# Kernel tuning notes

Hardware: AMD Instinct MI355X
Metric: run time of the kernel (lower is better)

## Reference

```python
import jax, jax.numpy as jnp
import numpy as np

D_MODEL = 1024
N_HEADS = 16
D_HEAD = D_MODEL // N_HEADS
D_FF = 4096
B, T = 2, 2048


def setup_inputs() -> dict:
    key = jax.random.key(0)
    ks = jax.random.split(key, 8)
    s = 0.02
    return {
        "x": jax.random.normal(ks[0], (B, T, D_MODEL), dtype=jnp.float32),
        "wq": jax.random.normal(ks[1], (D_MODEL, D_MODEL), dtype=jnp.float32) * s,
        "wk": jax.random.normal(ks[2], (D_MODEL, D_MODEL), dtype=jnp.float32) * s,
        "wv": jax.random.normal(ks[3], (D_MODEL, D_MODEL), dtype=jnp.float32) * s,
        "wo": jax.random.normal(ks[4], (D_MODEL, D_MODEL), dtype=jnp.float32) * s,
        "w1": jax.random.normal(ks[5], (D_FF, D_MODEL), dtype=jnp.float32) * s,
        "b1": jnp.zeros((D_FF,), dtype=jnp.float32),
        "w2": jax.random.normal(ks[6], (D_MODEL, D_FF), dtype=jnp.float32) * s,
        "b2": jnp.zeros((D_MODEL,), dtype=jnp.float32),
        "ln1_g": jnp.ones((D_MODEL,), dtype=jnp.float32),
        "ln1_b": jnp.zeros((D_MODEL,), dtype=jnp.float32),
        "ln2_g": jnp.ones((D_MODEL,), dtype=jnp.float32),
        "ln2_b": jnp.zeros((D_MODEL,), dtype=jnp.float32),
    }


def _layernorm(x, g, b, eps=1e-5):
    mu = jnp.mean(x, axis=-1, keepdims=True)
    var = jnp.mean(jnp.square(x - mu), axis=-1, keepdims=True)
    return (x - mu) * jax.lax.rsqrt(var + eps) * g + b


def reference(x, wq, wk, wv, wo, w1, b1, w2, b2, ln1_g, ln1_b, ln2_g, ln2_b):
    Bsz, Tlen, C = x.shape
    h = _layernorm(x, ln1_g, ln1_b)
    # torch Linear: y = h @ W^T ; reshape to [B, H, T, Dh]
    def proj(w):
        return (h @ w.T).reshape(Bsz, Tlen, N_HEADS, D_HEAD).transpose(0, 2, 1, 3)
    q, k, v = proj(wq), proj(wk), proj(wv)
    scores = jnp.einsum('bhqd,bhkd->bhqk', q, k) / np.sqrt(D_HEAD).astype(np.float32)
    p = jax.nn.softmax(scores.astype(jnp.float32), axis=-1).astype(scores.dtype)
    out = jnp.einsum('bhqk,bhkd->bhqd', p, v)
    out = out.transpose(0, 2, 1, 3).reshape(Bsz, Tlen, C)
    x = x + out @ wo.T
    h2 = _layernorm(x, ln2_g, ln2_b)
    ff = jax.nn.gelu(h2 @ w1.T + b1, approximate=False) @ w2.T + b2
    return x + ff
```

## Files before the change

kernel.cpp:

```cpp
#include <hip/hip_runtime.h>
#include <hip/hip_bf16.h>
#include <math.h>

#define DM   1024
#define NH   16
#define DH   64
#define DFF  4096
#define BB   2
#define TT   2048
#define MTOK (BB*TT)
#define QS   3072

typedef unsigned short u16;
typedef unsigned int   u32;
typedef __attribute__((ext_vector_type(8))) __bf16 bf16x8;
typedef __attribute__((ext_vector_type(4))) float  f32x4;

__device__ inline float bf2f(u16 u) { return __uint_as_float(((u32)u) << 16); }
__device__ inline u16 f2bf(float f) {
  u32 u = __float_as_uint(f);
  u += 0x7FFFu + ((u >> 16) & 1u);
  return (u16)(u >> 16);
}
__device__ inline u32 packtrunc(float lo, float hi) {
  return __builtin_amdgcn_perm(__float_as_uint(hi), __float_as_uint(lo), 0x07060302u);
}
__device__ inline float fexp2(float x) { return __builtin_amdgcn_exp2f(x); }

__device__ inline void gload_lds16(const void* g, void* l) {
  __builtin_amdgcn_global_load_lds(
      (const __attribute__((address_space(1))) void*)g,
      (__attribute__((address_space(3))) void*)l,
      16, 0, 0);
}

__global__ __launch_bounds__(256) void prep(
    const float* __restrict__ wq, const float* __restrict__ wk, const float* __restrict__ wv,
    const float* __restrict__ wo, const float* __restrict__ w1, const float* __restrict__ w2,
    const float* __restrict__ x, const float* __restrict__ g, const float* __restrict__ be,
    u16* __restrict__ wqkv_b, u16* __restrict__ wo_b, u16* __restrict__ w1_b,
    u16* __restrict__ w2_b, u16* __restrict__ h1)
{
  const int blk = blockIdx.x;
  if (blk < 12288) {
    const float* src; u16* dst; int idx;
    if (blk < 3072) {
      idx = blk * 256 + threadIdx.x;
      const int sel = idx >> 18;
      const int j = idx & 0x3FFFF;
      src = sel == 0 ? wq : (sel == 1 ? wk : wv);
      dst = wqkv_b;
      float4 v = ((const float4*)src)[j];
      ushort4 o; o.x = f2bf(v.x); o.y = f2bf(v.y); o.z = f2bf(v.z); o.w = f2bf(v.w);
      ((ushort4*)dst)[idx] = o;
      return;
    } else if (blk < 4096) { src = wo; dst = wo_b; idx = (blk - 3072) * 256 + threadIdx.x; }
    else if (blk < 8192)   { src = w1; dst = w1_b; idx = (blk - 4096) * 256 + threadIdx.x; }
    else                   { src = w2; dst = w2_b; idx = (blk - 8192) * 256 + threadIdx.x; }
    float4 v = ((const float4*)src)[idx];
    ushort4 o; o.x = f2bf(v.x); o.y = f2bf(v.y); o.z = f2bf(v.z); o.w = f2bf(v.w);
    ((ushort4*)dst)[idx] = o;
    return;
  }
  const int w = threadIdx.x >> 6, lane = threadIdx.x & 63;
  const int row = (blk - 12288) * 4 + w;
  const float4* xr = (const float4*)(x + (size_t)row * DM);
  float4 v[4];
  float s = 0.f, s2 = 0.f;
#pragma unroll
  for (int i = 0; i < 4; i++) {
    v[i] = xr[i * 64 + lane];
    s  += v[i].x + v[i].y + v[i].z + v[i].w;
    s2 += v[i].x * v[i].x + v[i].y * v[i].y + v[i].z * v[i].z + v[i].w * v[i].w;
  }
#pragma unroll
  for (int off = 32; off > 0; off >>= 1) {
    s  += __shfl_xor(s,  off);
    s2 += __shfl_xor(s2, off);
  }
  const float mu = s * (1.f / DM);
  const float rs = rsqrtf(s2 * (1.f / DM) - mu * mu + 1e-5f);
  u16* orow = h1 + (size_t)row * DM;
#pragma unroll
  for (int i = 0; i < 4; i++) {
    const float4 gg = ((const float4*)g)[i * 64 + lane];
    const float4 bb = ((const float4*)be)[i * 64 + lane];
    ushort4 o;
    o.x = f2bf((v[i].x - mu) * rs * gg.x + bb.x);
    o.y = f2bf((v[i].y - mu) * rs * gg.y + bb.y);
    o.z = f2bf((v[i].z - mu) * rs * gg.z + bb.z);
    o.w = f2bf((v[i].w - mu) * rs * gg.w + bb.w);
    ((ushort4*)orow)[i * 64 + lane] = o;
  }
}

__global__ __launch_bounds__(256) void ln_to_bf16(
    const float* __restrict__ x, const float* __restrict__ g, const float* __restrict__ be,
    u16* __restrict__ out)
{
  const int w = threadIdx.x >> 6, lane = threadIdx.x & 63;
  const int row = blockIdx.x * 4 + w;
  const float4* xr = (const float4*)(x + (size_t)row * DM);
  float4 v[4];
  float s = 0.f, s2 = 0.f;
#pragma unroll
  for (int i = 0; i < 4; i++) {
    v[i] = xr[i * 64 + lane];
    s  += v[i].x + v[i].y + v[i].z + v[i].w;
    s2 += v[i].x * v[i].x + v[i].y * v[i].y + v[i].z * v[i].z + v[i].w * v[i].w;
  }
#pragma unroll
  for (int off = 32; off > 0; off >>= 1) {
    s  += __shfl_xor(s,  off);
    s2 += __shfl_xor(s2, off);
  }
  const float mu = s * (1.f / DM);
  const float rs = rsqrtf(s2 * (1.f / DM) - mu * mu + 1e-5f);
  u16* orow = out + (size_t)row * DM;
#pragma unroll
  for (int i = 0; i < 4; i++) {
    const float4 gg = ((const float4*)g)[i * 64 + lane];
    const float4 bb = ((const float4*)be)[i * 64 + lane];
    ushort4 o;
    o.x = f2bf((v[i].x - mu) * rs * gg.x + bb.x);
    o.y = f2bf((v[i].y - mu) * rs * gg.y + bb.y);
    o.z = f2bf((v[i].z - mu) * rs * gg.z + bb.z);
    o.w = f2bf((v[i].w - mu) * rs * gg.w + bb.w);
    ((ushort4*)orow)[i * 64 + lane] = o;
  }
}

template <int EPI, int BN>
__global__ __launch_bounds__(256) void gemm_bt(
    const u16* __restrict__ A, const u16* __restrict__ Bw,
    int M, int N, int K,
    const float* __restrict__ bias, const float* __restrict__ resid,
    float* __restrict__ outF, u16* __restrict__ outB, float oscale, int scaleN)
{
  constexpr int NJ = BN / 32;
  __shared__ u16 As[128 * 64];
  __shared__ u16 Bs[BN * 64];

  const int tid  = threadIdx.x;
  const int w    = tid >> 6;
  const int lane = tid & 63;
  const int wr   = w >> 1, wc = w & 1;
  const int q    = lane >> 4;
  const int li   = lane & 15;
  const int rowBase = blockIdx.y * 128;
  const int colBase = blockIdx.x * BN;

  const int lr = lane >> 3;
  const int cs = (lane & 7) ^ lr;
  const u16* Abase = A  + (size_t)(rowBase + lr) * K + cs * 8;
  const u16* Bbase = Bw + (size_t)(colBase + lr) * K + cs * 8;

  f32x4 acc[4][NJ] = {};

  for (int k0 = 0; k0 < K; k0 += 64) {
    __syncthreads();
#pragma unroll
    for (int jj = 0; jj < 4; jj++) {
      const int rb = (w * 4 + jj) * 8;
      gload_lds16(Abase + (size_t)rb * K + k0, &As[rb * 64]);
    }
#pragma unroll
    for (int jj = 0; jj < NJ; jj++) {
      const int rb = (w * NJ + jj) * 8;
      gload_lds16(Bbase + (size_t)rb * K + k0, &Bs[rb * 64]);
    }
    __syncthreads();
#pragma unroll
    for (int kk = 0; kk < 2; kk++) {
      bf16x8 fa[4], fb[NJ];
      const int pos = (kk * 4 + q) ^ (li & 7);
#pragma unroll
      for (int i = 0; i < 4; i++) {
        const int row = wr * 64 + i * 16 + li;
        fa[i] = *(const bf16x8*)&As[row * 64 + pos * 8];
      }
#pragma unroll
      for (int j = 0; j < NJ; j++) {
        const int row = wc * (BN / 2) + j * 16 + li;
        fb[j] = *(const bf16x8*)&Bs[row * 64 + pos * 8];
      }
#pragma unroll
      for (int i = 0; i < 4; i++)
#pragma unroll
        for (int j = 0; j < NJ; j++)
          acc[i][j] = __builtin_amdgcn_mfma_f32_16x16x32_bf16(fa[i], fb[j], acc[i][j], 0, 0, 0);
    }
  }

#pragma unroll
  for (int i = 0; i < 4; i++) {
#pragma unroll
    for (int j = 0; j < NJ; j++) {
      const int col = colBase + wc * (BN / 2) + j * 16 + li;
      float bv = 0.f;
      if constexpr (EPI == 2 || EPI == 3) bv = bias[col];
#pragma unroll
      for (int r = 0; r < 4; r++) {
        const int row = rowBase + wr * 64 + i * 16 + q * 4 + r;
        float v = acc[i][j][r] + bv;
        if constexpr (EPI == 1 || EPI == 3) v += resid[(size_t)row * N + col];
        if constexpr (EPI == 2) {
          const float z = fexp2(-v * (2.302213f + 0.1029625f * v * v));
          v = v * __builtin_amdgcn_rcpf(1.f + z);
        }
        if constexpr (EPI == 0) {
          const float sc = (col < scaleN) ? oscale : 1.f;
          v *= sc;
        }
        if constexpr (EPI == 0 || EPI == 2) outB[(size_t)row * N + col] = f2bf(v);
        else                                outF[(size_t)row * N + col] = v;
      }
    }
  }
}

__global__ __launch_bounds__(256) void transpose_v(
    const u16* __restrict__ vq, u16* __restrict__ vt)
{
  __shared__ u16 t[64][72];
  const int bh = blockIdx.x, b = bh >> 4, h = bh & 15;
  const int t0 = blockIdx.y * 64;
  const int tid = threadIdx.x;
  const int r = tid >> 2, c = (tid & 3) * 16;
  const u16* src = vq + (size_t)(b * TT + t0 + r) * QS + h * DH + c;
#pragma unroll
  for (int i = 0; i < 4; i++)
    *(ushort4*)&t[r][c + i * 4] = ((const ushort4*)src)[i];
  __syncthreads();
  const int dh = tid >> 2, tt = (tid & 3) * 16;
  u16* dst = vt + ((size_t)bh * 64 + dh) * TT + t0 + tt;
#pragma unroll
  for (int i = 0; i < 4; i++) {
    ushort4 o;
    o.x = t[tt + i * 4 + 0][dh]; o.y = t[tt + i * 4 + 1][dh];
    o.z = t[tt + i * 4 + 2][dh]; o.w = t[tt + i * 4 + 3][dh];
    ((ushort4*)dst)[i] = o;
  }
}

__global__ __launch_bounds__(256) void attn_mfma(
    const u16* __restrict__ qb, const u16* __restrict__ kb,
    const u16* __restrict__ vt, u16* __restrict__ ob)
{
  __shared__ u16 Ks[2][64 * 64];
  __shared__ u16 Vs[2][64 * 64];
  __shared__ u16 Sh[4 * 32 * 72];

  const int tid = threadIdx.x, w = tid >> 6, lane = tid & 63;
  const int q = lane >> 4, li = lane & 15;
  const int bh = blockIdx.x, b = bh >> 4, h = bh & 15;
  const int q0 = blockIdx.y * 128;
  const int lr8 = lane >> 3, lc8 = lane & 7;

#pragma unroll
  for (int jj = 0; jj < 4; jj++) {
    const int rb = w * 32 + jj * 8;
    const int row = rb + lr8;
    const int cs = lc8 ^ (row & 7);
    gload_lds16(qb + (size_t)(b * TT + q0 + row) * QS + h * DH + cs * 8,
                &Sh[rb * 64]);
  }
  __syncthreads();

  bf16x8 qf[2][2];
#pragma unroll
  for (int n = 0; n < 2; n++)
#pragma unroll
    for (int kk = 0; kk < 2; kk++) {
      const int row = w * 32 + n * 16 + li;
      const int pos = (kk * 4 + q) ^ (li & 7);
      qf[n][kk] = *(const bf16x8*)&Sh[row * 64 + pos * 8];
    }

  auto stage = [&](int buf, int kt) {
#pragma unroll
    for (int half = 0; half < 2; half++) {
      const int rb = w * 16 + half * 8;
      const int row = rb + lr8;
      const int cs = lc8 ^ (row & 7);
      gload_lds16(kb + (size_t)(b * TT + kt + row) * QS + h * DH + cs * 8,
                  &Ks[buf][rb * 64]);
      gload_lds16(vt + ((size_t)bh * 64 + row) * TT + kt + cs * 8,
                  &Vs[buf][rb * 64]);
    }
  };

  f32x4 ot[4][2] = {};
  float lsum[2] = {0.f, 0.f};
  u16* Pw = &Sh[w * 32 * 72];

  stage(0, 0);
  for (int it = 0; it < TT / 64; it++) {
    __syncthreads();
    if (it + 1 < TT / 64) stage((it + 1) & 1, (it + 1) * 64);
    const u16* Kc = Ks[it & 1];
    const u16* Vc = Vs[it & 1];

    f32x4 st[4][2] = {};
#pragma unroll
    for (int kk = 0; kk < 2; kk++)
#pragma unroll
      for (int i = 0; i < 4; i++) {
        const int pos = (kk * 4 + q) ^ (li & 7);
        const bf16x8 kf = *(const bf16x8*)&Kc[(i * 16 + li) * 64 + pos * 8];
#pragma unroll
        for (int n = 0; n < 2; n++)
          st[i][n] = __builtin_amdgcn_mfma_f32_16x16x32_bf16(kf, qf[n][kk], st[i][n], 0, 0, 0);
      }

    u32 pk[4][2][2];
#pragma unroll
    for (int i = 0; i < 4; i++)
#pragma unroll
      for (int n = 0; n < 2; n++) {
        const float p0 = fexp2(st[i][n][0]);
        const float p1 = fexp2(st[i][n][1]);
        const float p2 = fexp2(st[i][n][2]);
        const float p3 = fexp2(st[i][n][3]);
        lsum[n] += (p0 + p1) + (p2 + p3);
        pk[i][n][0] = packtrunc(p0, p1);
        pk[i][n][1] = packtrunc(p2, p3);
      }

#pragma unroll
    for (int i = 0; i < 4; i++)
#pragma unroll
      for (int n = 0; n < 2; n++) {
        const int a = (n * 16 + li) * 72 + i * 16 + q * 4;
        *(u32*)&Pw[a]     = pk[i][n][0];
        *(u32*)&Pw[a + 2] = pk[i][n][1];
      }

#pragma unroll
    for (int kk = 0; kk < 2; kk++) {
      bf16x8 pf[2];
#pragma unroll
      for (int n = 0; n < 2; n++)
        pf[n] = *(const bf16x8*)&Pw[(n * 16 + li) * 72 + kk * 32 + q * 8];
#pragma unroll
      for (int m = 0; m < 4; m++) {
        const int pos = (kk * 4 + q) ^ (li & 7);
        const bf16x8 vf = *(const bf16x8*)&Vc[(m * 16 + li) * 64 + pos * 8];
#pragma unroll
        for (int n = 0; n < 2; n++)
          ot[m][n] = __builtin_amdgcn_mfma_f32_16x16x32_bf16(vf, pf[n], ot[m][n], 0, 0, 0);
      }
    }
  }

  float inv[2];
#pragma unroll
  for (int n = 0; n < 2; n++) {
    float s = lsum[n];
    s += __shfl_xor(s, 16);
    s += __shfl_xor(s, 32);
    inv[n] = 1.f / s;
  }
#pragma unroll
  for (int m = 0; m < 4; m++)
#pragma unroll
    for (int n = 0; n < 2; n++) {
      const int a = (n * 16 + li) * 72 + m * 16 + q * 4;
      *(u32*)&Pw[a]     = packtrunc(ot[m][n][0] * inv[n], ot[m][n][1] * inv[n]);
      *(u32*)&Pw[a + 2] = packtrunc(ot[m][n][2] * inv[n], ot[m][n][3] * inv[n]);
    }
#pragma unroll
  for (int pass = 0; pass < 4; pass++) {
    const int row = pass * 8 + lr8;
    const bf16x8 v = *(const bf16x8*)&Pw[row * 72 + lc8 * 8];
    const int token = q0 + w * 32 + row;
    *(bf16x8*)(ob + ((size_t)(b * TT + token) * NH + h) * DH + lc8 * 8) = v;
  }
}

extern "C" void kernel_launch(void* const* d_in, const int* in_sizes, int n_in,
                              void* d_out, int out_size, void* d_ws, size_t ws_size,
                              hipStream_t stream) {
  const float* x    = (const float*)d_in[0];
  const float* wq   = (const float*)d_in[1];
  const float* wk   = (const float*)d_in[2];
  const float* wv   = (const float*)d_in[3];
  const float* wo   = (const float*)d_in[4];
  const float* w1   = (const float*)d_in[5];
  const float* b1   = (const float*)d_in[6];
  const float* w2   = (const float*)d_in[7];
  const float* b2   = (const float*)d_in[8];
  const float* ln1g = (const float*)d_in[9];
  const float* ln1b = (const float*)d_in[10];
  const float* ln2g = (const float*)d_in[11];
  const float* ln2b = (const float*)d_in[12];

  size_t off = 0;
  char* base = (char*)d_ws;
  auto alloc = [&](size_t bytes) { void* p = base + off; off += bytes; return p; };

  u16* wqkv_b = (u16*)alloc((size_t)3 * DM * DM * 2);
  u16* wo_b   = (u16*)alloc((size_t)DM * DM * 2);
  u16* w1_b   = (u16*)alloc((size_t)DFF * DM * 2);
  u16* w2_b   = (u16*)alloc((size_t)DM * DFF * 2);
  u16* h1     = (u16*)alloc((size_t)MTOK * DM * 2);
  u16* qkvb   = (u16*)alloc((size_t)MTOK * QS * 2);
  u16* attn   = (u16*)alloc((size_t)MTOK * DM * 2);
  u16* h2     = (u16*)alloc((size_t)MTOK * DM * 2);
  u16* ff1    = (u16*)alloc((size_t)MTOK * DFF * 2);
  float* xmid = (float*)alloc((size_t)MTOK * DM * 4);
  u16* vtb    = ff1;
  (void)ws_size; (void)in_sizes; (void)n_in; (void)out_size;

  prep<<<13312, 256, 0, stream>>>(wq, wk, wv, wo, w1, w2, x, ln1g, ln1b,
                                  wqkv_b, wo_b, w1_b, w2_b, h1);

  const float QSCALE = 0.125f * 1.44269504088896340736f;
  gemm_bt<0, 128><<<dim3(QS / 128, MTOK / 128), 256, 0, stream>>>(
      h1, wqkv_b, MTOK, QS, DM, nullptr, nullptr, nullptr, qkvb, QSCALE, DM);

  transpose_v<<<dim3(BB * NH, TT / 64), 256, 0, stream>>>(qkvb + 2 * DM, vtb);
  attn_mfma<<<dim3(BB * NH, TT / 128), 256, 0, stream>>>(qkvb, qkvb + DM, vtb, attn);

  gemm_bt<1, 64><<<dim3(DM / 64, MTOK / 128), 256, 0, stream>>>(
      attn, wo_b, MTOK, DM, DM, nullptr, x, xmid, nullptr, 1.f, 0);

  ln_to_bf16<<<MTOK / 4, 256, 0, stream>>>(xmid, ln2g, ln2b, h2);

  gemm_bt<2, 128><<<dim3(DFF / 128, MTOK / 128), 256, 0, stream>>>(
      h2, w1_b, MTOK, DFF, DM, b1, nullptr, nullptr, ff1, 1.f, 0);
  gemm_bt<3, 64><<<dim3(DM / 64, MTOK / 128), 256, 0, stream>>>(
      ff1, w2_b, MTOK, DM, DFF, b2, xmid, (float*)d_out, nullptr, 1.f, 0);
}
```

Before: 355.5 us.

## Double-buffer GEMM LDS tiles with K-step 32 and one barrier per iteration

```diff
diff --git a/kernel.cpp b/kernel.cpp
--- a/kernel.cpp
+++ b/kernel.cpp
@@ -138,8 +138,8 @@
     float* __restrict__ outF, u16* __restrict__ outB, float oscale, int scaleN)
 {
   constexpr int NJ = BN / 32;
-  __shared__ u16 As[128 * 64];
-  __shared__ u16 Bs[BN * 64];
+  __shared__ u16 As[2][128 * 32];
+  __shared__ u16 Bs[2][BN * 32];
 
   const int tid  = threadIdx.x;
   const int w    = tid >> 6;
@@ -150,46 +150,64 @@
   const int rowBase = blockIdx.y * 128;
   const int colBase = blockIdx.x * BN;
 
-  const int lr = lane >> 3;
-  const int cs = (lane & 7) ^ lr;
-  const u16* Abase = A  + (size_t)(rowBase + lr) * K + cs * 8;
-  const u16* Bbase = Bw + (size_t)(colBase + lr) * K + cs * 8;
+  const int lrow = lane >> 2;
+  const int lchk = lane & 3;
+
+  const u16* Asrc[2];
+  const u16* Bsrc[NJ / 2 > 0 ? NJ / 2 : 1];
+  int Abase_lds[2], Bbase_lds[2];
+#pragma unroll
+  for (int jj = 0; jj < 2; jj++) {
+    const int row = w * 32 + jj * 16 + lrow;
+    const int cs = lchk ^ ((row >> 1) & 3);
+    Asrc[jj] = A + (size_t)(rowBase + row) * K + cs * 8;
+    Abase_lds[jj] = (w * 32 + jj * 16) * 32;
+  }
+#pragma unroll
+  for (int jj = 0; jj < NJ / 2; jj++) {
+    const int row = w * (16 * NJ / 2) + jj * 16 + lrow;
+    const int cs = lchk ^ ((row >> 1) & 3);
+    Bsrc[jj] = Bw + (size_t)(colBase + row) * K + cs * 8;
+    Bbase_lds[jj] = (w * (16 * NJ / 2) + jj * 16) * 32;
+  }
+
+  auto stage = [&](int buf, int k0) {
+#pragma unroll
+    for (int jj = 0; jj < 2; jj++)
+      gload_lds16(Asrc[jj] + k0, &As[buf][Abase_lds[jj]]);
+#pragma unroll
+    for (int jj = 0; jj < NJ / 2; jj++)
+      gload_lds16(Bsrc[jj] + k0, &Bs[buf][Bbase_lds[jj]]);
+  };
 
   f32x4 acc[4][NJ] = {};
 
-  for (int k0 = 0; k0 < K; k0 += 64) {
+  stage(0, 0);
+  const int NIT = K / 32;
+  for (int it = 0; it < NIT; it++) {
     __syncthreads();
-#pragma unroll
-    for (int jj = 0; jj < 4; jj++) {
-      const int rb = (w * 4 + jj) * 8;
-      gload_lds16(Abase + (size_t)rb * K + k0, &As[rb * 64]);
-    }
-#pragma unroll
-    for (int jj = 0; jj < NJ; jj++) {
-      const int rb = (w * NJ + jj) * 8;
-      gload_lds16(Bbase + (size_t)rb * K + k0, &Bs[rb * 64]);
-    }
-    __syncthreads();
-#pragma unroll
-    for (int kk = 0; kk < 2; kk++) {
-      bf16x8 fa[4], fb[NJ];
-      const int pos = (kk * 4 + q) ^ (li & 7);
-#pragma unroll
-      for (int i = 0; i < 4; i++) {
-        const int row = wr * 64 + i * 16 + li;
-        fa[i] = *(const bf16x8*)&As[row * 64 + pos * 8];
-      }
-#pragma unroll
-      for (int j = 0; j < NJ; j++) {
-        const int row = wc * (BN / 2) + j * 16 + li;
-        fb[j] = *(const bf16x8*)&Bs[row * 64 + pos * 8];
-      }
-#pragma unroll
-      for (int i = 0; i < 4; i++)
-#pragma unroll
-        for (int j = 0; j < NJ; j++)
-          acc[i][j] = __builtin_amdgcn_mfma_f32_16x16x32_bf16(fa[i], fb[j], acc[i][j], 0, 0, 0);
-    }
+    if (it + 1 < NIT) stage((it + 1) & 1, (it + 1) * 32);
+    const u16* Ac = As[it & 1];
+    const u16* Bc = Bs[it & 1];
+
+    bf16x8 fa[4], fb[NJ];
+#pragma unroll
+    for (int i = 0; i < 4; i++) {
+      const int row = wr * 64 + i * 16 + li;
+      const int pos = q ^ ((row >> 1) & 3);
+      fa[i] = *(const bf16x8*)&Ac[row * 32 + pos * 8];
+    }
+#pragma unroll
+    for (int j = 0; j < NJ; j++) {
+      const int row = wc * (BN / 2) + j * 16 + li;
+      const int pos = q ^ ((row >> 1) & 3);
+      fb[j] = *(const bf16x8*)&Bc[row * 32 + pos * 8];
+    }
+#pragma unroll
+    for (int i = 0; i < 4; i++)
+#pragma unroll
+      for (int j = 0; j < NJ; j++)
+        acc[i][j] = __builtin_amdgcn_mfma_f32_16x16x32_bf16(fa[i], fb[j], acc[i][j], 0, 0, 0);
   }
 
 #pragma unroll
```

Result: no change. 362.3 us (+1.9%).

## Split-K the N=1024 GEMMs and fuse partial-sum reduction with residual/LayerNorm

Applied to the files above, without the earlier changes.

```diff
diff --git a/kernel.cpp b/kernel.cpp
--- a/kernel.cpp
+++ b/kernel.cpp
@@ -94,18 +94,26 @@
   }
 }
 
-__global__ __launch_bounds__(256) void ln_to_bf16(
-    const float* __restrict__ x, const float* __restrict__ g, const float* __restrict__ be,
-    u16* __restrict__ out)
-{
+__global__ __launch_bounds__(256) void reduce_ln(
+    const float* __restrict__ x, const float* __restrict__ P,
+    const float* __restrict__ g, const float* __restrict__ be,
+    float* __restrict__ xmid, u16* __restrict__ h2)
+{
+  const float* P0 = P;
+  const float* P1 = P + (size_t)MTOK * DM;
   const int w = threadIdx.x >> 6, lane = threadIdx.x & 63;
   const int row = blockIdx.x * 4 + w;
-  const float4* xr = (const float4*)(x + (size_t)row * DM);
+  const size_t roff = (size_t)row * DM;
   float4 v[4];
   float s = 0.f, s2 = 0.f;
 #pragma unroll
   for (int i = 0; i < 4; i++) {
-    v[i] = xr[i * 64 + lane];
+    const float4 a = ((const float4*)(x  + roff))[i * 64 + lane];
+    const float4 p = ((const float4*)(P0 + roff))[i * 64 + lane];
+    const float4 qv = ((const float4*)(P1 + roff))[i * 64 + lane];
+    v[i].x = a.x + p.x + qv.x; v[i].y = a.y + p.y + qv.y;
+    v[i].z = a.z + p.z + qv.z; v[i].w = a.w + p.w + qv.w;
+    ((float4*)(xmid + roff))[i * 64 + lane] = v[i];
     s  += v[i].x + v[i].y + v[i].z + v[i].w;
     s2 += v[i].x * v[i].x + v[i].y * v[i].y + v[i].z * v[i].z + v[i].w * v[i].w;
   }
@@ -116,7 +124,7 @@
   }
   const float mu = s * (1.f / DM);
   const float rs = rsqrtf(s2 * (1.f / DM) - mu * mu + 1e-5f);
-  u16* orow = out + (size_t)row * DM;
+  u16* orow = h2 + roff;
 #pragma unroll
   for (int i = 0; i < 4; i++) {
     const float4 gg = ((const float4*)g)[i * 64 + lane];
@@ -130,12 +138,29 @@
   }
 }
 
+__global__ __launch_bounds__(256) void reduce_out(
+    const float* __restrict__ Q, const float* __restrict__ xmid,
+    const float* __restrict__ b2, float* __restrict__ out)
+{
+  const float* Q0 = Q;
+  const float* Q1 = Q + (size_t)MTOK * DM;
+  const int i = blockIdx.x * 256 + threadIdx.x;
+  const float4 a = ((const float4*)xmid)[i];
+  const float4 p = ((const float4*)Q0)[i];
+  const float4 qv = ((const float4*)Q1)[i];
+  const float4 bb = ((const float4*)b2)[i & (DM / 4 - 1)];
+  float4 o;
+  o.x = a.x + p.x + qv.x + bb.x; o.y = a.y + p.y + qv.y + bb.y;
+  o.z = a.z + p.z + qv.z + bb.z; o.w = a.w + p.w + qv.w + bb.w;
+  ((float4*)out)[i] = o;
+}
+
 template <int EPI, int BN>
 __global__ __launch_bounds__(256) void gemm_bt(
     const u16* __restrict__ A, const u16* __restrict__ Bw,
     int M, int N, int K,
-    const float* __restrict__ bias, const float* __restrict__ resid,
-    float* __restrict__ outF, u16* __restrict__ outB, float oscale, int scaleN)
+    const float* __restrict__ bias,
+    u16* __restrict__ outB, float oscale, int scaleN)
 {
   constexpr int NJ = BN / 32;
   __shared__ u16 As[128 * 64];
@@ -198,12 +223,11 @@
     for (int j = 0; j < NJ; j++) {
       const int col = colBase + wc * (BN / 2) + j * 16 + li;
       float bv = 0.f;
-      if constexpr (EPI == 2 || EPI == 3) bv = bias[col];
+      if constexpr (EPI == 2) bv = bias[col];
 #pragma unroll
       for (int r = 0; r < 4; r++) {
         const int row = rowBase + wr * 64 + i * 16 + q * 4 + r;
         float v = acc[i][j][r] + bv;
-        if constexpr (EPI == 1 || EPI == 3) v += resid[(size_t)row * N + col];
         if constexpr (EPI == 2) {
           const float z = fexp2(-v * (2.302213f + 0.1029625f * v * v));
           v = v * __builtin_amdgcn_rcpf(1.f + z);
@@ -212,11 +236,83 @@
           const float sc = (col < scaleN) ? oscale : 1.f;
           v *= sc;
         }
-        if constexpr (EPI == 0 || EPI == 2) outB[(size_t)row * N + col] = f2bf(v);
-        else                                outF[(size_t)row * N + col] = v;
-      }
-    }
-  }
+        outB[(size_t)row * N + col] = f2bf(v);
+      }
+    }
+  }
+}
+
+__global__ __launch_bounds__(256) void gemm_sk(
+    const u16* __restrict__ A, const u16* __restrict__ Bw,
+    int N, int K, int KLEN, float* __restrict__ P)
+{
+  __shared__ u16 As[128 * 64];
+  __shared__ u16 Bs[64 * 64];
+
+  const int tid  = threadIdx.x;
+  const int w    = tid >> 6;
+  const int lane = tid & 63;
+  const int wr   = w >> 1, wc = w & 1;
+  const int q    = lane >> 4;
+  const int li   = lane & 15;
+  const int rowBase = blockIdx.y * 128;
+  const int colBase = blockIdx.x * 64;
+  const int koff = blockIdx.z * KLEN;
+
+  const int lr = lane >> 3;
+  const int cs = (lane & 7) ^ lr;
+  const u16* Abase = A  + (size_t)(rowBase + lr) * K + koff + cs * 8;
+  const u16* Bbase = Bw + (size_t)(colBase + lr) * K + koff + cs * 8;
+
+  f32x4 acc[4][2] = {};
+
+  for (int k0 = 0; k0 < KLEN; k0 += 64) {
+    __syncthreads();
+#pragma unroll
+    for (int jj = 0; jj < 4; jj++) {
+      const int rb = (w * 4 + jj) * 8;
+      gload_lds16(Abase + (size_t)rb * K + k0, &As[rb * 64]);
+    }
+#pragma unroll
+    for (int jj = 0; jj < 2; jj++) {
+      const int rb = (w * 2 + jj) * 8;
+      gload_lds16(Bbase + (size_t)rb * K + k0, &Bs[rb * 64]);
+    }
+    __syncthreads();
+#pragma unroll
+    for (int kk = 0; kk < 2; kk++) {
+      bf16x8 fa[4], fb[2];
+      const int pos = (kk * 4 + q) ^ (li & 7);
+#pragma unroll
+      for (int i = 0; i < 4; i++) {
+        const int row = wr * 64 + i * 16 + li;
+        fa[i] = *(const bf16x8*)&As[row * 64 + pos * 8];
+      }
+#pragma unroll
+      for (int j = 0; j < 2; j++) {
+        const int row = wc * 32 + j * 16 + li;
+        fb[j] = *(const bf16x8*)&Bs[row * 64 + pos * 8];
+      }
+#pragma unroll
+      for (int i = 0; i < 4; i++)
+#pragma unroll
+        for (int j = 0; j < 2; j++)
+          acc[i][j] = __builtin_amdgcn_mfma_f32_16x16x32_bf16(fa[i], fb[j], acc[i][j], 0, 0, 0);
+    }
+  }
+
+  float* Pz = P + (size_t)blockIdx.z * MTOK * DM;
+#pragma unroll
+  for (int i = 0; i < 4; i++)
+#pragma unroll
+    for (int j = 0; j < 2; j++) {
+      const int col = colBase + wc * 32 + j * 16 + li;
+#pragma unroll
+      for (int r = 0; r < 4; r++) {
+        const int row = rowBase + wr * 64 + i * 16 + q * 4 + r;
+        Pz[(size_t)row * N + col] = acc[i][j][r];
+      }
+    }
 }
 
 __global__ __launch_bounds__(256) void transpose_v(
@@ -410,6 +506,8 @@
   u16* ff1    = (u16*)alloc((size_t)MTOK * DFF * 2);
   float* xmid = (float*)alloc((size_t)MTOK * DM * 4);
   u16* vtb    = ff1;
+  float* woP  = (float*)ff1;
+  float* ff2P = (float*)h1;
   (void)ws_size; (void)in_sizes; (void)n_in; (void)out_size;
 
   prep<<<13312, 256, 0, stream>>>(wq, wk, wv, wo, w1, w2, x, ln1g, ln1b,
@@ -417,18 +515,18 @@
 
   const float QSCALE = 0.125f * 1.44269504088896340736f;
   gemm_bt<0, 128><<<dim3(QS / 128, MTOK / 128), 256, 0, stream>>>(
-      h1, wqkv_b, MTOK, QS, DM, nullptr, nullptr, nullptr, qkvb, QSCALE, DM);
+      h1, wqkv_b, MTOK, QS, DM, nullptr, qkvb, QSCALE, DM);
 
   transpose_v<<<dim3(BB * NH, TT / 64), 256, 0, stream>>>(qkvb + 2 * DM, vtb);
   attn_mfma<<<dim3(BB * NH, TT / 128), 256, 0, stream>>>(qkvb, qkvb + DM, vtb, attn);
 
-  gemm_bt<1, 64><<<dim3(DM / 64, MTOK / 128), 256, 0, stream>>>(
-      attn, wo_b, MTOK, DM, DM, nullptr, x, xmid, nullptr, 1.f, 0);
-
-  ln_to_bf16<<<MTOK / 4, 256, 0, stream>>>(xmid, ln2g, ln2b, h2);
+  gemm_sk<<<dim3(DM / 64, MTOK / 128, 2), 256, 0, stream>>>(
+      attn, wo_b, DM, DM, DM / 2, woP);
+  reduce_ln<<<MTOK / 4, 256, 0, stream>>>(x, woP, ln2g, ln2b, xmid, h2);
 
   gemm_bt<2, 128><<<dim3(DFF / 128, MTOK / 128), 256, 0, stream>>>(
-      h2, w1_b, MTOK, DFF, DM, b1, nullptr, nullptr, ff1, 1.f, 0);
-  gemm_bt<3, 64><<<dim3(DM / 64, MTOK / 128), 256, 0, stream>>>(
-      ff1, w2_b, MTOK, DM, DFF, b2, xmid, (float*)d_out, nullptr, 1.f, 0);
-}
+      h2, w1_b, MTOK, DFF, DM, b1, ff1, 1.f, 0);
+  gemm_sk<<<dim3(DM / 64, MTOK / 128, 2), 256, 0, stream>>>(
+      ff1, w2_b, DM, DFF, DFF / 2, ff2P);
+  reduce_out<<<MTOK * DM / 4 / 256, 256, 0, stream>>>(ff2P, xmid, b2, (float*)d_out);
+}
```

New measurement: 350.0 us. Within noise of the previous version (-1.6%).
